# Kernel tuning notes

Hardware: AMD Instinct MI355X
Metric: run time of the kernel (lower is better)

Reference implementation:

```python
import jax, jax.numpy as jnp
import numpy as np

N = 250_000          # num nodes
E = 2_000_000        # undirected edges -> 2E directed edges
C = 2                # num_class
POT = 0.95           # self potential
THRESH = 1e-6
MAX_ITERS = 10


def setup_inputs() -> dict:
    key = jax.random.key(0)
    k1, k2, k3 = jax.random.split(key, 3)
    u = jax.random.randint(k1, (E,), 0, N)
    v = jax.random.randint(k2, (E,), 0, N)
    # directed edge list: first E edges u->v, next E edges v->u
    src_nodes = jnp.concatenate([u, v]).astype(jnp.int64)
    dst_nodes = jnp.concatenate([v, u]).astype(jnp.int64)
    # reverse-edge index: edge i (<E) reverses to i+E and vice versa
    ar = jnp.arange(E, dtype=jnp.int64)
    rev_edges = jnp.concatenate([ar + E, ar])
    # strictly positive class priors, rows sum to 1
    priors = jax.nn.softmax(jax.random.normal(k3, (N, C), dtype=jnp.float32), axis=1)
    return {"priors": priors, "src_nodes": src_nodes,
            "dst_nodes": dst_nodes, "rev_edges": rev_edges}


def _potential_matrix(dtype):
    off = (1.0 - POT) / C * (C - 1)
    diag = POT / C
    P = jnp.full((C, C), off, dtype=dtype)
    return P.at[jnp.arange(C), jnp.arange(C)].set(diag)


def reference(priors, src_nodes, dst_nodes, rev_edges):
    P = _potential_matrix(priors.dtype)
    log_priors = jnp.log(priors)
    n_dir = src_nodes.shape[0]  # 2E directed edges
    messages0 = jnp.full((n_dir, C), 0.5, dtype=priors.dtype)

    def update_messages(messages, beliefs):
        # gather beliefs at edge sources, divide by reverse messages, CxC matmul
        m = (beliefs[src_nodes] / messages[rev_edges]) @ P  # [2E, C]
        return m / jnp.sum(m, axis=1, keepdims=True)

    def compute_beliefs(messages):
        b = log_priors.at[dst_nodes].add(jnp.log(messages))  # scatter-add
        return jax.nn.softmax(b, axis=1)

    def cond(state):
        i, beliefs, messages, diff = state
        return jnp.logical_and(i < MAX_ITERS, diff >= THRESH)

    def body(state):
        i, beliefs, messages, _ = state
        new_m = update_messages(messages, beliefs)
        new_b = compute_beliefs(new_m)
        diff = jnp.max(jnp.abs(new_b - beliefs))
        return (i + 1, new_b, new_m, diff)

    init = (jnp.array(0, jnp.int32), priors, messages0,
            jnp.array(jnp.inf, priors.dtype))
    _, beliefs, _, _ = jax.lax.while_loop(cond, body, init)
    return beliefs
```

## Files before the change

kernel.cpp:

```cpp
#include <hip/hip_runtime.h>
#include <hip/hip_fp16.h>


#define POT_D 0.475f
#define POT_O 0.025f

constexpr int BKT_SHIFT = 8;
constexpr int BKT_NODES = 1 << BKT_SHIFT;
constexpr int GB = 512;
constexpr int GB2 = 128;
constexpr int ITEMS = GB / 64;
constexpr int FB = 512;
constexpr int T = 9;

__device__ __forceinline__ float pot_logit(float x) {
  float t = __expf(-fabsf(x));
  float v = __logf((POT_D + POT_O * t) / (POT_O + POT_D * t));
  return copysignf(v, x);
}

__global__ void init_nodes(const float* __restrict__ priors, float* __restrict__ lpd,
                           __half* __restrict__ z0, int N) {
  int n = blockIdx.x * blockDim.x + threadIdx.x;
  if (n < N) {
    float2 p = reinterpret_cast<const float2*>(priors)[n];
    float l = __logf(p.x) - __logf(p.y);
    lpd[n] = l;
    z0[n] = __float2half(l);
  }
}

__global__ void zero_msgs(unsigned* __restrict__ Lpack, unsigned* __restrict__ Lrpack, int Mw) {
  int i = blockIdx.x * blockDim.x + threadIdx.x;
  if (i < Mw) { Lpack[i] = 0u; Lrpack[i] = 0u; }
}

__global__ void rank_kernel(const int* __restrict__ dst, int* __restrict__ blkhist,
                            int* __restrict__ rnk, int M, int NB, int CH) {
  extern __shared__ int h[];
  for (int i = threadIdx.x; i < NB; i += blockDim.x) h[i] = 0;
  __syncthreads();
  int s = blockIdx.x * CH, e1 = min(s + CH, M);
  for (int e = s + threadIdx.x; e < e1; e += blockDim.x)
    rnk[e] = atomicAdd(&h[dst[e] >> BKT_SHIFT], 1);
  __syncthreads();
  for (int i = threadIdx.x; i < NB; i += blockDim.x)
    blkhist[(size_t)i * GB + blockIdx.x] = h[i];
}

__global__ void colscan_kernel(int* __restrict__ blkhist, int* __restrict__ deg, int NB) {
  int wave = (blockIdx.x * blockDim.x + threadIdx.x) >> 6;
  int lane = threadIdx.x & 63;
  if (wave >= NB) return;
  int* row = blkhist + (size_t)wave * GB;
  int v[ITEMS];
  int s = 0;
#pragma unroll
  for (int j = 0; j < ITEMS; ++j) { v[j] = row[ITEMS * lane + j]; s += v[j]; }
  int tot = s;
  for (int off = 1; off < 64; off <<= 1) {
    int t = __shfl_up(tot, off, 64);
    if (lane >= off) tot += t;
  }
  int excl = tot - s;
#pragma unroll
  for (int j = 0; j < ITEMS; ++j) { int t = v[j]; row[ITEMS * lane + j] = excl; excl += t; }
  if (lane == 63) deg[wave] = tot;
}

__global__ void scan_kernel(const int* __restrict__ deg, int* __restrict__ base,
                            int NB, int M) {
  __shared__ int s[1024];
  __shared__ int carry;
  int tid = threadIdx.x;
  if (tid == 0) carry = 0;
  __syncthreads();
  for (int c = 0; c < NB; c += 1024) {
    int v = (c + tid < NB) ? deg[c + tid] : 0;
    s[tid] = v;
    __syncthreads();
    for (int off = 1; off < 1024; off <<= 1) {
      int t = (tid >= off) ? s[tid - off] : 0;
      __syncthreads();
      s[tid] += t;
      __syncthreads();
    }
    if (c + tid < NB) base[c + tid] = carry + s[tid] - v;
    __syncthreads();
    if (tid == 0) carry += s[1023];
    __syncthreads();
  }
  if (tid == 0) base[NB] = M;
}

__global__ void place_kernel(const int* __restrict__ dst, const int* __restrict__ blkhist,
                             const int* __restrict__ base, const int* __restrict__ rnk,
                             int* __restrict__ posof, int M, int NB, int CH) {
  extern __shared__ int cur[];
  for (int i = threadIdx.x; i < NB; i += blockDim.x)
    cur[i] = base[i] + blkhist[(size_t)i * GB + blockIdx.x];
  __syncthreads();
  int s = blockIdx.x * CH, e1 = min(s + CH, M);
  for (int e = s + threadIdx.x; e < e1; e += blockDim.x)
    posof[e] = cur[dst[e] >> BKT_SHIFT] + rnk[e];
}

__global__ void pass2_kernel(const int* __restrict__ src, const int* __restrict__ dst,
                             const int* __restrict__ posof, unsigned* __restrict__ g3,
                             int M, int CH2) {
  int s = blockIdx.x * CH2, e1 = min(s + CH2, M);
  for (int e = s + threadIdx.x; e < e1; e += blockDim.x) {
    unsigned loc = (unsigned)(dst[e] & (BKT_NODES - 1));
    g3[posof[e]] = (loc << 18) | (unsigned)src[e];
  }
}

__global__ __launch_bounds__(FB, 4) void iter_kernel(
    const unsigned* __restrict__ g3, const int* __restrict__ base,
    const float* __restrict__ lpd, const __half* __restrict__ zin,
    __half* __restrict__ zout, __half* __restrict__ L, __half* __restrict__ Lr, int N) {
  __shared__ float zb[BKT_NODES];
  __shared__ float zdl[BKT_NODES];
  const int tid = threadIdx.x;
  const int b = blockIdx.x;
  const int rs = base[b], re = base[b + 1];
  const int node = (b << BKT_SHIFT) + tid;
  if (tid < BKT_NODES) {
    zb[tid] = 0.0f;
    zdl[tid] = (node < N) ? __half2float(zin[node]) : 0.0f;
  }
  __syncthreads();
  if (re > rs) {
    const int k0 = rs + tid;
    unsigned w[T];
    float lr[T], l[T], zs[T];
#pragma unroll
    for (int j = 0; j < T; ++j) {
      int k = min(k0 + j * FB, re - 1);
      w[j] = g3[k];
      lr[j] = __half2float(Lr[k]);
      l[j] = __half2float(L[k]);
    }
#pragma unroll
    for (int j = 0; j < T; ++j)
      zs[j] = __half2float(zin[w[j] & 0x3FFFFu]);
#pragma unroll
    for (int j = 0; j < T; ++j) {
      int k = k0 + j * FB;
      float Ln = pot_logit(zs[j] - lr[j]);
      float Lrn = pot_logit(zdl[w[j] >> 18] - l[j]);
      if (k < re) {
        atomicAdd(&zb[w[j] >> 18], Ln);
        L[k] = __float2half(Ln);
        Lr[k] = __float2half(Lrn);
      }
    }
    for (int k = k0 + T * FB; k < re; k += FB) {
      unsigned w2 = g3[k];
      float Ln = pot_logit(__half2float(zin[w2 & 0x3FFFFu]) - __half2float(Lr[k]));
      float Lrn = pot_logit(zdl[w2 >> 18] - __half2float(L[k]));
      atomicAdd(&zb[w2 >> 18], Ln);
      L[k] = __float2half(Ln);
      Lr[k] = __float2half(Lrn);
    }
  }
  __syncthreads();
  if (tid < BKT_NODES && node < N)
    zout[node] = __float2half(lpd[node] + zb[tid]);
}

__global__ __launch_bounds__(FB, 4) void out_kernel(
    const unsigned* __restrict__ g3, const int* __restrict__ base,
    const float* __restrict__ lpd, const __half* __restrict__ zin,
    const __half* __restrict__ Lr, float2* __restrict__ out, int N) {
  __shared__ float zb[BKT_NODES];
  const int tid = threadIdx.x;
  const int b = blockIdx.x;
  const int rs = base[b], re = base[b + 1];
  const int node = (b << BKT_SHIFT) + tid;
  if (tid < BKT_NODES) zb[tid] = 0.0f;
  __syncthreads();
  if (re > rs) {
    const int k0 = rs + tid;
    unsigned w[T];
    float lr[T], zs[T];
#pragma unroll
    for (int j = 0; j < T; ++j) {
      int k = min(k0 + j * FB, re - 1);
      w[j] = g3[k];
      lr[j] = __half2float(Lr[k]);
    }
#pragma unroll
    for (int j = 0; j < T; ++j)
      zs[j] = __half2float(zin[w[j] & 0x3FFFFu]);
#pragma unroll
    for (int j = 0; j < T; ++j)
      if (k0 + j * FB < re) atomicAdd(&zb[w[j] >> 18], pot_logit(zs[j] - lr[j]));
    for (int k = k0 + T * FB; k < re; k += FB) {
      unsigned w2 = g3[k];
      atomicAdd(&zb[w2 >> 18], pot_logit(__half2float(zin[w2 & 0x3FFFFu]) - __half2float(Lr[k])));
    }
  }
  __syncthreads();
  if (tid < BKT_NODES && node < N) {
    float z = lpd[node] + zb[tid];
    float p = 1.0f / (1.0f + __expf(-z));
    out[node] = make_float2(p, 1.0f - p);
  }
}

extern "C" void kernel_launch(void* const* d_in, const int* in_sizes, int n_in,
                              void* d_out, int out_size, void* d_ws, size_t ws_size,
                              hipStream_t stream) {
  const float* priors = (const float*)d_in[0];
  const int* src = (const int*)d_in[1];
  const int* dst = (const int*)d_in[2];
  int N = in_sizes[0] / 2;
  int M = in_sizes[1];
  int NB = (N + BKT_NODES - 1) / BKT_NODES;
  int CH = (M + GB - 1) / GB;
  int CH2 = (M + GB2 - 1) / GB2;

  float* ws = (float*)d_ws;
  float* lpd = ws;
  unsigned* g3 = (unsigned*)(ws + N);
  int* rnk = (int*)(ws + N + (size_t)M);
  int* posof = (int*)(ws + N + 2 * (size_t)M);
  __half* L = (__half*)(ws + N + 3 * (size_t)M);
  __half* Lr = L + M;
  __half* zA = Lr + M;
  __half* zB = zA + N;
  int* blkhist = (int*)(zB + N);
  int* deg = blkhist + (size_t)NB * GB;
  int* base = deg + NB;
  float2* outp = (float2*)d_out;

  const int B = 256;
  init_nodes<<<(N + B - 1) / B, B, 0, stream>>>(priors, lpd, zA, N);
  zero_msgs<<<(M + B - 1) / B, B, 0, stream>>>((unsigned*)L, (unsigned*)Lr, M / 2);
  rank_kernel<<<GB, B, NB * sizeof(int), stream>>>(dst, blkhist, rnk, M, NB, CH);
  colscan_kernel<<<(NB * 64 + B - 1) / B, B, 0, stream>>>(blkhist, deg, NB);
  scan_kernel<<<1, 1024, 0, stream>>>(deg, base, NB, M);
  place_kernel<<<GB, B, NB * sizeof(int), stream>>>(dst, blkhist, base, rnk, posof, M, NB, CH);
  pass2_kernel<<<GB2, 512, 0, stream>>>(src, dst, posof, g3, M, CH2);

  __half* zs[2] = {zA, zB};
  for (int t = 1; t <= 9; ++t)
    iter_kernel<<<NB, FB, 0, stream>>>(g3, base, lpd, zs[(t - 1) & 1], zs[t & 1],
                                       L, Lr, N);
  out_kernel<<<NB, FB, 0, stream>>>(g3, base, lpd, zB, Lr, outp, N);
}
```

Baseline: 511.1 us.

## Interleave message pairs and fuse rank/place/scatter into atomic counting-sort scatter

Stores forward and reverse messages interleaved as half2 so each edge reads and writes one 4-byte word instead of two separate arrays. Replaces the rank/place/pass2 chain with a histogram pass plus a single scatter kernel that claims slots with shared-memory atomics, removing the rnk and posof arrays and their global traffic. It also shrinks the single-block scan to one wavefront using shuffles and vectorises the zeroing. Edge order within a bucket becomes nondeterministic, which changes the floating-point summation order, and each scatter block covers two histogram chunks by reading only the first chunk's offset.

After: 476.5 us. 1.07x faster.

```diff
diff --git a/kernel.cpp b/kernel.cpp
--- a/kernel.cpp
+++ b/kernel.cpp
@@ -8,8 +8,8 @@
 constexpr int BKT_SHIFT = 8;
 constexpr int BKT_NODES = 1 << BKT_SHIFT;
 constexpr int GB = 512;
-constexpr int GB2 = 128;
 constexpr int ITEMS = GB / 64;
+constexpr int GB3 = 256;
 constexpr int FB = 512;
 constexpr int T = 9;
 
@@ -30,19 +30,19 @@
   }
 }
 
-__global__ void zero_msgs(unsigned* __restrict__ Lpack, unsigned* __restrict__ Lrpack, int Mw) {
+__global__ void zero_msgs(uint4* __restrict__ P4, int Mq) {
   int i = blockIdx.x * blockDim.x + threadIdx.x;
-  if (i < Mw) { Lpack[i] = 0u; Lrpack[i] = 0u; }
-}
-
-__global__ void rank_kernel(const int* __restrict__ dst, int* __restrict__ blkhist,
-                            int* __restrict__ rnk, int M, int NB, int CH) {
+  if (i < Mq) P4[i] = make_uint4(0, 0, 0, 0);
+}
+
+__global__ void hist_kernel(const int* __restrict__ dst, int* __restrict__ blkhist,
+                            int M, int NB, int CH) {
   extern __shared__ int h[];
   for (int i = threadIdx.x; i < NB; i += blockDim.x) h[i] = 0;
   __syncthreads();
   int s = blockIdx.x * CH, e1 = min(s + CH, M);
   for (int e = s + threadIdx.x; e < e1; e += blockDim.x)
-    rnk[e] = atomicAdd(&h[dst[e] >> BKT_SHIFT], 1);
+    atomicAdd(&h[dst[e] >> BKT_SHIFT], 1);
   __syncthreads();
   for (int i = threadIdx.x; i < NB; i += blockDim.x)
     blkhist[(size_t)i * GB + blockIdx.x] = h[i];
@@ -70,55 +70,40 @@
 
 __global__ void scan_kernel(const int* __restrict__ deg, int* __restrict__ base,
                             int NB, int M) {
-  __shared__ int s[1024];
-  __shared__ int carry;
-  int tid = threadIdx.x;
-  if (tid == 0) carry = 0;
-  __syncthreads();
-  for (int c = 0; c < NB; c += 1024) {
-    int v = (c + tid < NB) ? deg[c + tid] : 0;
-    s[tid] = v;
-    __syncthreads();
-    for (int off = 1; off < 1024; off <<= 1) {
-      int t = (tid >= off) ? s[tid - off] : 0;
-      __syncthreads();
-      s[tid] += t;
-      __syncthreads();
-    }
-    if (c + tid < NB) base[c + tid] = carry + s[tid] - v;
-    __syncthreads();
-    if (tid == 0) carry += s[1023];
-    __syncthreads();
-  }
-  if (tid == 0) base[NB] = M;
-}
-
-__global__ void place_kernel(const int* __restrict__ dst, const int* __restrict__ blkhist,
-                             const int* __restrict__ base, const int* __restrict__ rnk,
-                             int* __restrict__ posof, int M, int NB, int CH) {
+  int lane = threadIdx.x;
+  int carry = 0;
+  for (int c = 0; c < NB; c += 64) {
+    int v = (c + lane < NB) ? deg[c + lane] : 0;
+    int s = v;
+    for (int off = 1; off < 64; off <<= 1) {
+      int t = __shfl_up(s, off, 64);
+      if (lane >= off) s += t;
+    }
+    if (c + lane < NB) base[c + lane] = carry + s - v;
+    carry += __shfl(s, 63, 64);
+  }
+  if (lane == 0) base[NB] = M;
+}
+
+__global__ void scatterg3_kernel(const int* __restrict__ src, const int* __restrict__ dst,
+                                 const int* __restrict__ blkhist, const int* __restrict__ base,
+                                 unsigned* __restrict__ g3, int M, int NB, int CH) {
   extern __shared__ int cur[];
   for (int i = threadIdx.x; i < NB; i += blockDim.x)
-    cur[i] = base[i] + blkhist[(size_t)i * GB + blockIdx.x];
-  __syncthreads();
-  int s = blockIdx.x * CH, e1 = min(s + CH, M);
-  for (int e = s + threadIdx.x; e < e1; e += blockDim.x)
-    posof[e] = cur[dst[e] >> BKT_SHIFT] + rnk[e];
-}
-
-__global__ void pass2_kernel(const int* __restrict__ src, const int* __restrict__ dst,
-                             const int* __restrict__ posof, unsigned* __restrict__ g3,
-                             int M, int CH2) {
-  int s = blockIdx.x * CH2, e1 = min(s + CH2, M);
+    cur[i] = base[i] + blkhist[(size_t)i * GB + 2 * blockIdx.x];
+  __syncthreads();
+  int s = blockIdx.x * 2 * CH, e1 = min(s + 2 * CH, M);
   for (int e = s + threadIdx.x; e < e1; e += blockDim.x) {
-    unsigned loc = (unsigned)(dst[e] & (BKT_NODES - 1));
-    g3[posof[e]] = (loc << 18) | (unsigned)src[e];
+    int d = dst[e];
+    int pos = atomicAdd(&cur[d >> BKT_SHIFT], 1);
+    g3[pos] = ((unsigned)(d & (BKT_NODES - 1)) << 18) | (unsigned)src[e];
   }
 }
 
 __global__ __launch_bounds__(FB, 4) void iter_kernel(
     const unsigned* __restrict__ g3, const int* __restrict__ base,
     const float* __restrict__ lpd, const __half* __restrict__ zin,
-    __half* __restrict__ zout, __half* __restrict__ L, __half* __restrict__ Lr, int N) {
+    __half* __restrict__ zout, __half2* __restrict__ P, int N) {
   __shared__ float zb[BKT_NODES];
   __shared__ float zdl[BKT_NODES];
   const int tid = threadIdx.x;
@@ -133,13 +118,14 @@
   if (re > rs) {
     const int k0 = rs + tid;
     unsigned w[T];
-    float lr[T], l[T], zs[T];
+    float l[T], lr[T], zs[T];
 #pragma unroll
     for (int j = 0; j < T; ++j) {
       int k = min(k0 + j * FB, re - 1);
       w[j] = g3[k];
-      lr[j] = __half2float(Lr[k]);
-      l[j] = __half2float(L[k]);
+      __half2 pv = P[k];
+      l[j] = __half2float(__low2half(pv));
+      lr[j] = __half2float(__high2half(pv));
     }
 #pragma unroll
     for (int j = 0; j < T; ++j)
@@ -151,17 +137,16 @@
       float Lrn = pot_logit(zdl[w[j] >> 18] - l[j]);
       if (k < re) {
         atomicAdd(&zb[w[j] >> 18], Ln);
-        L[k] = __float2half(Ln);
-        Lr[k] = __float2half(Lrn);
+        P[k] = __halves2half2(__float2half(Ln), __float2half(Lrn));
       }
     }
     for (int k = k0 + T * FB; k < re; k += FB) {
       unsigned w2 = g3[k];
-      float Ln = pot_logit(__half2float(zin[w2 & 0x3FFFFu]) - __half2float(Lr[k]));
-      float Lrn = pot_logit(zdl[w2 >> 18] - __half2float(L[k]));
+      __half2 pv = P[k];
+      float Ln = pot_logit(__half2float(zin[w2 & 0x3FFFFu]) - __half2float(__high2half(pv)));
+      float Lrn = pot_logit(zdl[w2 >> 18] - __half2float(__low2half(pv)));
       atomicAdd(&zb[w2 >> 18], Ln);
-      L[k] = __float2half(Ln);
-      Lr[k] = __float2half(Lrn);
+      P[k] = __halves2half2(__float2half(Ln), __float2half(Lrn));
     }
   }
   __syncthreads();
@@ -172,7 +157,7 @@
 __global__ __launch_bounds__(FB, 4) void out_kernel(
     const unsigned* __restrict__ g3, const int* __restrict__ base,
     const float* __restrict__ lpd, const __half* __restrict__ zin,
-    const __half* __restrict__ Lr, float2* __restrict__ out, int N) {
+    const __half2* __restrict__ P, float2* __restrict__ out, int N) {
   __shared__ float zb[BKT_NODES];
   const int tid = threadIdx.x;
   const int b = blockIdx.x;
@@ -188,7 +173,7 @@
     for (int j = 0; j < T; ++j) {
       int k = min(k0 + j * FB, re - 1);
       w[j] = g3[k];
-      lr[j] = __half2float(Lr[k]);
+      lr[j] = __half2float(__high2half(P[k]));
     }
 #pragma unroll
     for (int j = 0; j < T; ++j)
@@ -198,7 +183,8 @@
       if (k0 + j * FB < re) atomicAdd(&zb[w[j] >> 18], pot_logit(zs[j] - lr[j]));
     for (int k = k0 + T * FB; k < re; k += FB) {
       unsigned w2 = g3[k];
-      atomicAdd(&zb[w2 >> 18], pot_logit(__half2float(zin[w2 & 0x3FFFFu]) - __half2float(Lr[k])));
+      atomicAdd(&zb[w2 >> 18],
+                pot_logit(__half2float(zin[w2 & 0x3FFFFu]) - __half2float(__high2half(P[k]))));
     }
   }
   __syncthreads();
@@ -219,16 +205,12 @@
   int M = in_sizes[1];
   int NB = (N + BKT_NODES - 1) / BKT_NODES;
   int CH = (M + GB - 1) / GB;
-  int CH2 = (M + GB2 - 1) / GB2;
 
   float* ws = (float*)d_ws;
   float* lpd = ws;
   unsigned* g3 = (unsigned*)(ws + N);
-  int* rnk = (int*)(ws + N + (size_t)M);
-  int* posof = (int*)(ws + N + 2 * (size_t)M);
-  __half* L = (__half*)(ws + N + 3 * (size_t)M);
-  __half* Lr = L + M;
-  __half* zA = Lr + M;
+  __half2* P = (__half2*)(ws + N + (size_t)M);
+  __half* zA = (__half*)(P + M);
   __half* zB = zA + N;
   int* blkhist = (int*)(zB + N);
   int* deg = blkhist + (size_t)NB * GB;
@@ -237,16 +219,14 @@
 
   const int B = 256;
   init_nodes<<<(N + B - 1) / B, B, 0, stream>>>(priors, lpd, zA, N);
-  zero_msgs<<<(M + B - 1) / B, B, 0, stream>>>((unsigned*)L, (unsigned*)Lr, M / 2);
-  rank_kernel<<<GB, B, NB * sizeof(int), stream>>>(dst, blkhist, rnk, M, NB, CH);
+  zero_msgs<<<(M / 4 + B - 1) / B, B, 0, stream>>>((uint4*)P, M / 4);
+  hist_kernel<<<GB, B, NB * sizeof(int), stream>>>(dst, blkhist, M, NB, CH);
   colscan_kernel<<<(NB * 64 + B - 1) / B, B, 0, stream>>>(blkhist, deg, NB);
-  scan_kernel<<<1, 1024, 0, stream>>>(deg, base, NB, M);
-  place_kernel<<<GB, B, NB * sizeof(int), stream>>>(dst, blkhist, base, rnk, posof, M, NB, CH);
-  pass2_kernel<<<GB2, 512, 0, stream>>>(src, dst, posof, g3, M, CH2);
+  scan_kernel<<<1, 64, 0, stream>>>(deg, base, NB, M);
+  scatterg3_kernel<<<GB3, 512, NB * sizeof(int), stream>>>(src, dst, blkhist, base, g3, M, NB, CH);
 
   __half* zs[2] = {zA, zB};
   for (int t = 1; t <= 9; ++t)
-    iter_kernel<<<NB, FB, 0, stream>>>(g3, base, lpd, zs[(t - 1) & 1], zs[t & 1],
-                                       L, Lr, N);
-  out_kernel<<<NB, FB, 0, stream>>>(g3, base, lpd, zB, Lr, outp, N);
-}
+    iter_kernel<<<NB, FB, 0, stream>>>(g3, base, lpd, zs[(t - 1) & 1], zs[t & 1], P, N);
+  out_kernel<<<NB, FB, 0, stream>>>(g3, base, lpd, zB, P, outp, N);
+}
```
